# Optimization experiments

Hardware: AMD Instinct MI355X
Metric: run time of the kernel (lower is better)

The kernel has to match this reference:

```python
import jax, jax.numpy as jnp
import numpy as np

V_SIZE = 128000  # vocab size (v_size init arg)


def setup_inputs() -> dict:
    key = jax.random.key(0)
    k1, k2 = jax.random.split(key)
    # per-position scores -> weighting_scheme (softmax over seq dim)
    w_es = jax.random.normal(k1, (256, 2048), dtype=jnp.float32)
    # instance['x']: token ids in [0, v_size)
    x = jax.random.randint(k2, (256, 2048), 0, V_SIZE, dtype=jnp.int64)
    return {"w_es": w_es, "x": x}


def reference(w_es, x):
    # weighting_scheme(indices, w_es, instance): softmax over sequence positions
    weights = jax.nn.softmax(w_es, axis=-1)          # [B, S]
    B, S = weights.shape
    rows = jnp.arange(B)[:, None]                    # [B, 1] broadcast against [B, S]
    # scatter: w_a[b, x[b, i]] = weights[b, i]  (vectorized index_put)
    w_a = jnp.zeros((B, V_SIZE), dtype=weights.dtype).at[rows, x].set(weights)
    return (w_a, weights)
```

## Files before the change

### kernel.cpp

```cpp
#include <hip/hip_runtime.h>

#define BATCH 256
#define SEQ   2048
#define VOCAB 128000
#define HASH  4096
#define CHUNK 4096
#define CPR   32
#define CAP   128

typedef float v2f __attribute__((ext_vector_type(2)));
typedef int   v2i __attribute__((ext_vector_type(2)));
typedef float v4f __attribute__((ext_vector_type(4)));
typedef int   v4i __attribute__((ext_vector_type(4)));

__global__ __launch_bounds__(1024, 4)
void rowprep_kernel(const float* __restrict__ w_es,
                    const int*   __restrict__ x,
                    float* __restrict__ w_out,
                    int*   __restrict__ counts,
                    int2*  __restrict__ pairs)
{
    __shared__ int   key [HASH];
    __shared__ int   maxi[HASH];
    __shared__ int   cnt [CPR];
    __shared__ float redm[16], reds[16];

    const int r = blockIdx.x;
    const int t = threadIdx.x;
    const int lane = t & 63;
    const int wid  = t >> 6;

    for (int j = t; j < HASH; j += 1024) { key[j] = -1; maxi[j] = -1; }
    if (t < CPR) cnt[t] = 0;

    const float* rowp = w_es + (size_t)r * SEQ;
    const v2f a = ((const v2f*)rowp)[t];
    const int* xrow = x + (size_t)r * SEQ;
    const v2i xt = ((const v2i*)xrow)[t];

    float m = fmaxf(a.x, a.y);
    #pragma unroll
    for (int off = 32; off > 0; off >>= 1)
        m = fmaxf(m, __shfl_down(m, off, 64));
    if (lane == 0) redm[wid] = m;
    __syncthreads();
    #pragma unroll
    for (int j = 0; j < 16; ++j) m = fmaxf(m, redm[j]);

    float e0 = __expf(a.x - m), e1 = __expf(a.y - m);
    float s = e0 + e1;
    #pragma unroll
    for (int off = 32; off > 0; off >>= 1)
        s += __shfl_down(s, off, 64);
    if (lane == 0) reds[wid] = s;
    __syncthreads();
    s = 0.0f;
    #pragma unroll
    for (int j = 0; j < 16; ++j) s += reds[j];

    const float inv = 1.0f / s;
    float w[2] = { e0 * inv, e1 * inv };

    float* wrow = w_out + (size_t)r * SEQ;
    v2f wv; wv.x = w[0]; wv.y = w[1];
    ((v2f*)wrow)[t] = wv;

    int tok[2] = { xt.x, xt.y };
    int idx[2] = { 2 * t, 2 * t + 1 };

    int slot[2];
    #pragma unroll
    for (int k = 0; k < 2; ++k) {
        unsigned h = (((unsigned)tok[k] * 2654435761u) >> 16) & (HASH - 1);
        int sl = (int)h;
        while (true) {
            int prev = atomicCAS(&key[sl], -1, tok[k]);
            if (prev == -1 || prev == tok[k]) break;
            sl = (sl + 1) & (HASH - 1);
        }
        slot[k] = sl;
        atomicMax(&maxi[sl], idx[k]);
    }
    __syncthreads();

    #pragma unroll
    for (int k = 0; k < 2; ++k) {
        if (maxi[slot[k]] == idx[k]) {
            int c   = tok[k] >> 12;
            int pos = atomicAdd(&cnt[c], 1);
            if (pos < CAP)
                pairs[(size_t)(r * CPR + c) * CAP + pos] =
                    make_int2(tok[k] & (CHUNK - 1), __float_as_int(w[k]));
        }
    }
    __syncthreads();
    if (t < CPR) counts[r * CPR + t] = min(cnt[t], CAP);
}

__global__ __launch_bounds__(256)
void fillscatter_kernel(const int*  __restrict__ counts,
                        const int2* __restrict__ pairs,
                        float* __restrict__ w_a)
{
    const int bid = blockIdx.x;
    const int r = bid >> 5;
    const int c = bid & (CPR - 1);
    const int base = c * CHUNK;
    const int cnt  = (VOCAB - base < CHUNK) ? (VOCAB - base) : CHUNK;
    const int cnt4 = cnt >> 2;
    const int t = threadIdx.x;

    int2 pr = make_int2(0, 0);
    if (t < CAP) pr = pairs[(size_t)bid * CAP + t];
    const int n = counts[bid];

    float* gp = w_a + (size_t)r * VOCAB + base;
    const v4f z = (v4f)0.0f;
    for (int j = t; j < cnt4; j += 256)
        ((v4f*)gp)[j] = z;

    __syncthreads();

    if (t < n)
        gp[pr.x] = __int_as_float(pr.y);
}

extern "C" void kernel_launch(void* const* d_in, const int* in_sizes, int n_in,
                              void* d_out, int out_size, void* d_ws, size_t ws_size,
                              hipStream_t stream) {
    const float* w_es = (const float*)d_in[0];
    const int*   x    = (const int*)d_in[1];

    float* out  = (float*)d_out;
    float* w_a  = out;
    float* w    = out + (size_t)BATCH * VOCAB;

    int*  counts = (int*)d_ws;
    int2* pairs  = (int2*)((char*)d_ws + BATCH * CPR * sizeof(int));

    rowprep_kernel    <<<BATCH,       1024, 0, stream>>>(w_es, x, w, counts, pairs);
    fillscatter_kernel<<<BATCH * CPR, 256,  0, stream>>>(counts, pairs, w_a);
}
```

Measured before the change: 147.3 us.

## Fuse softmax, zero-fill and scatter into a single per-row kernel

Replaces the two-kernel pipeline with one kernel per row. The old pipeline bucketed deduplicated (token, weight) pairs into a workspace, then ran a chunked fill-and-scatter kernel. Now each 1024-thread block zeroes its whole 128000-entry output row, computes the softmax and last-writer dedup in shared memory, and writes the winning weights straight into the row. This removes the workspace round trip, the per-chunk capacity limit and the second launch. The cost is that the full output fill is spread over only 256 blocks instead of 8192, which may limit write bandwidth.

```diff
diff --git a/kernel.cpp b/kernel.cpp
--- a/kernel.cpp
+++ b/kernel.cpp
@@ -4,25 +4,19 @@
 #define SEQ   2048
 #define VOCAB 128000
 #define HASH  4096
-#define CHUNK 4096
-#define CPR   32
-#define CAP   128
 
 typedef float v2f __attribute__((ext_vector_type(2)));
 typedef int   v2i __attribute__((ext_vector_type(2)));
 typedef float v4f __attribute__((ext_vector_type(4)));
-typedef int   v4i __attribute__((ext_vector_type(4)));
 
 __global__ __launch_bounds__(1024, 4)
-void rowprep_kernel(const float* __restrict__ w_es,
-                    const int*   __restrict__ x,
-                    float* __restrict__ w_out,
-                    int*   __restrict__ counts,
-                    int2*  __restrict__ pairs)
+void fused_row_kernel(const float* __restrict__ w_es,
+                      const int*   __restrict__ x,
+                      float* __restrict__ w_a,
+                      float* __restrict__ w_out)
 {
     __shared__ int   key [HASH];
     __shared__ int   maxi[HASH];
-    __shared__ int   cnt [CPR];
     __shared__ float redm[16], reds[16];
 
     const int r = blockIdx.x;
@@ -30,13 +24,20 @@
     const int lane = t & 63;
     const int wid  = t >> 6;
 
-    for (int j = t; j < HASH; j += 1024) { key[j] = -1; maxi[j] = -1; }
-    if (t < CPR) cnt[t] = 0;
+    float* grow = w_a + (size_t)r * VOCAB;
+    {
+        const v4f z = (v4f)0.0f;
+        #pragma unroll 4
+        for (int j = t; j < (VOCAB / 4); j += 1024)
+            ((v4f*)grow)[j] = z;
+    }
 
     const float* rowp = w_es + (size_t)r * SEQ;
     const v2f a = ((const v2f*)rowp)[t];
     const int* xrow = x + (size_t)r * SEQ;
     const v2i xt = ((const v2i*)xrow)[t];
+
+    for (int j = t; j < HASH; j += 1024) { key[j] = -1; maxi[j] = -1; }
 
     float m = fmaxf(a.x, a.y);
     #pragma unroll
@@ -59,15 +60,16 @@
     for (int j = 0; j < 16; ++j) s += reds[j];
 
     const float inv = 1.0f / s;
-    float w[2] = { e0 * inv, e1 * inv };
+    float w0 = e0 * inv, w1 = e1 * inv;
 
-    float* wrow = w_out + (size_t)r * SEQ;
-    v2f wv; wv.x = w[0]; wv.y = w[1];
-    ((v2f*)wrow)[t] = wv;
+    {
+        v2f wv; wv.x = w0; wv.y = w1;
+        ((v2f*)(w_out + (size_t)r * SEQ))[t] = wv;
+    }
 
     int tok[2] = { xt.x, xt.y };
     int idx[2] = { 2 * t, 2 * t + 1 };
-
+    float wv2[2] = { w0, w1 };
     int slot[2];
     #pragma unroll
     for (int k = 0; k < 2; ++k) {
@@ -81,48 +83,13 @@
         slot[k] = sl;
         atomicMax(&maxi[sl], idx[k]);
     }
+
     __syncthreads();
 
     #pragma unroll
-    for (int k = 0; k < 2; ++k) {
-        if (maxi[slot[k]] == idx[k]) {
-            int c   = tok[k] >> 12;
-            int pos = atomicAdd(&cnt[c], 1);
-            if (pos < CAP)
-                pairs[(size_t)(r * CPR + c) * CAP + pos] =
-                    make_int2(tok[k] & (CHUNK - 1), __float_as_int(w[k]));
-        }
-    }
-    __syncthreads();
-    if (t < CPR) counts[r * CPR + t] = min(cnt[t], CAP);
-}
-
-__global__ __launch_bounds__(256)
-void fillscatter_kernel(const int*  __restrict__ counts,
-                        const int2* __restrict__ pairs,
-                        float* __restrict__ w_a)
-{
-    const int bid = blockIdx.x;
-    const int r = bid >> 5;
-    const int c = bid & (CPR - 1);
-    const int base = c * CHUNK;
-    const int cnt  = (VOCAB - base < CHUNK) ? (VOCAB - base) : CHUNK;
-    const int cnt4 = cnt >> 2;
-    const int t = threadIdx.x;
-
-    int2 pr = make_int2(0, 0);
-    if (t < CAP) pr = pairs[(size_t)bid * CAP + t];
-    const int n = counts[bid];
-
-    float* gp = w_a + (size_t)r * VOCAB + base;
-    const v4f z = (v4f)0.0f;
-    for (int j = t; j < cnt4; j += 256)
-        ((v4f*)gp)[j] = z;
-
-    __syncthreads();
-
-    if (t < n)
-        gp[pr.x] = __int_as_float(pr.y);
+    for (int k = 0; k < 2; ++k)
+        if (maxi[slot[k]] == idx[k])
+            grow[tok[k]] = wv2[k];
 }
 
 extern "C" void kernel_launch(void* const* d_in, const int* in_sizes, int n_in,
@@ -135,9 +102,5 @@
     float* w_a  = out;
     float* w    = out + (size_t)BATCH * VOCAB;
 
-    int*  counts = (int*)d_ws;
-    int2* pairs  = (int2*)((char*)d_ws + BATCH * CPR * sizeof(int));
-
-    rowprep_kernel    <<<BATCH,       1024, 0, stream>>>(w_es, x, w, counts, pairs);
-    fillscatter_kernel<<<BATCH * CPR, 256,  0, stream>>>(counts, pairs, w_a);
+    fused_row_kernel<<<BATCH, 1024, 0, stream>>>(w_es, x, w_a, w);
 }
```

Measured after the change: 143.0 us. -2.9%, faster.
